# Performance work log

Hardware: AMD Instinct MI355X
Metric: run time of the kernel (lower is better)

The kernel has to match this reference:

```python
import math
import jax, jax.numpy as jnp
import numpy as np

BATCH, SEQ, D_MODEL, NUM_HEADS = 4, 2048, 1024, 16
D_K = D_MODEL // NUM_HEADS


def setup_inputs() -> dict:
    key = jax.random.key(0)
    ks = jax.random.split(key, 11)
    s = 0.02
    inp = {
        'encodings_q': jax.random.normal(ks[0], (BATCH, SEQ, D_MODEL), jnp.float32),
        'encodings_k': jax.random.normal(ks[1], (BATCH, SEQ, D_MODEL), jnp.float32),
        'encodings_v': jax.random.normal(ks[2], (BATCH, SEQ, D_MODEL), jnp.float32),
        # causal mask: True = masked out (matches masked_fill semantics)
        'mask': jnp.broadcast_to(jnp.triu(jnp.ones((SEQ, SEQ), bool), k=1),
                                 (BATCH, SEQ, SEQ)),
        'Wq': jax.random.normal(ks[3], (D_MODEL, D_MODEL), jnp.float32) * s,
        'bq': jnp.zeros((D_MODEL,), jnp.float32),
        'Wk': jax.random.normal(ks[4], (D_MODEL, D_MODEL), jnp.float32) * s,
        'bk': jnp.zeros((D_MODEL,), jnp.float32),
        'Wv': jax.random.normal(ks[5], (D_MODEL, D_MODEL), jnp.float32) * s,
        'bv': jnp.zeros((D_MODEL,), jnp.float32),
        'Wo': jax.random.normal(ks[6], (D_MODEL, D_MODEL), jnp.float32) * s,
        'bo': jnp.zeros((D_MODEL,), jnp.float32),
    }
    return inp


def reference(encodings_q, encodings_k, encodings_v, mask,
              Wq, bq, Wk, bk, Wv, bv, Wo, bo):
    B, S, D = encodings_q.shape
    H, Dk = NUM_HEADS, D_K
    # projections (nn.Linear: x @ W.T + b), split heads -> (B, H, S, Dk)
    q = (encodings_q @ Wq.T + bq).reshape(B, S, H, Dk).transpose(0, 2, 1, 3)
    k = (encodings_k @ Wk.T + bk).reshape(B, S, H, Dk).transpose(0, 2, 1, 3)
    v = (encodings_v @ Wv.T + bv).reshape(B, S, H, Dk).transpose(0, 2, 1, 3)
    scores = jnp.einsum('bhqd,bhkd->bhqk', q, k) / math.sqrt(Dk)
    # mask dim == 3 -> unsqueeze head dim; masked_fill(mask, -1e9)
    scores = jnp.where(mask[:, None, :, :], jnp.float32(-1e9), scores)
    weights = jax.nn.softmax(scores, axis=-1)
    attn = jnp.einsum('bhqk,bhkd->bhqd', weights, v)
    attn = attn.transpose(0, 2, 1, 3).reshape(B, S, D)
    return attn @ Wo.T + bo
```

## Files before the change

kernel.cpp:

```cpp
#include <hip/hip_runtime.h>
#include <hip/hip_bf16.h>
#include <cstdint>

typedef __bf16 bf16;
typedef bf16  bf16x4 __attribute__((ext_vector_type(4)));
typedef bf16  bf16x8 __attribute__((ext_vector_type(8)));
typedef float f32x4  __attribute__((ext_vector_type(4)));

#define MFMA16(a, b, c) __builtin_amdgcn_mfma_f32_16x16x32_bf16((a), (b), (c), 0, 0, 0)

constexpr int BATCH = 4;
constexpr int SEQ   = 2048;
constexpr int DM    = 1024;
constexpr int NH    = 16;
constexpr int DK    = 64;

constexpr float QSCALE = 0.125f * 1.44269504088896340736f;

__device__ __forceinline__ void gld_lds16(const void* g, void* l) {
    __builtin_amdgcn_global_load_lds(
        (const __attribute__((address_space(1))) unsigned int*)(uintptr_t)g,
        (__attribute__((address_space(3))) unsigned int*)(uintptr_t)l,
        16, 0, 0);
}

__device__ __forceinline__ bf16x8 cvt8(const float* __restrict__ p) {
    f32x4 a = *(const f32x4*)p;
    f32x4 b = *(const f32x4*)(p + 4);
    bf16x8 r;
    r[0] = (bf16)a[0]; r[1] = (bf16)a[1]; r[2] = (bf16)a[2]; r[3] = (bf16)a[3];
    r[4] = (bf16)b[0]; r[5] = (bf16)b[1]; r[6] = (bf16)b[2]; r[7] = (bf16)b[3];
    return r;
}

__global__ __launch_bounds__(256)
void cvt_all(const float* __restrict__ xq, const float* __restrict__ xk,
             const float* __restrict__ xv,
             const float* __restrict__ wq, const float* __restrict__ wk,
             const float* __restrict__ wv, const float* __restrict__ wo,
             bf16* __restrict__ X3, bf16* __restrict__ WB)
{
    const int bid = blockIdx.x;
    const float* s;
    bf16* d;
    int local;
    if (bid < 12288) {
        const int which = bid >> 12;
        local = bid & 4095;
        s = (which == 0) ? xq : (which == 1) ? xk : xv;
        d = X3 + (size_t)which * ((size_t)BATCH * SEQ * DM);
    } else {
        const int b2 = bid - 12288;
        const int which = b2 >> 9;
        local = b2 & 511;
        s = (which == 0) ? wq : (which == 1) ? wk : (which == 2) ? wv : wo;
        d = WB + (size_t)which * (size_t)(DM * DM);
    }
    const size_t i = ((size_t)local * 256 + threadIdx.x) * 8;
    *(bf16x8*)(d + i) = cvt8(s + i);
}

__global__ __launch_bounds__(256)
void cvt_x(const float* __restrict__ src, bf16* __restrict__ dst) {
    const size_t i = ((size_t)blockIdx.x * 256 + threadIdx.x) * 8;
    *(bf16x8*)(dst + i) = cvt8(src + i);
}

__global__ __launch_bounds__(256)
void cvt_w4(const float* __restrict__ s0, const float* __restrict__ s1,
            const float* __restrict__ s2, const float* __restrict__ s3,
            bf16* __restrict__ dst) {
    const float* s = (blockIdx.y == 0) ? s0 : (blockIdx.y == 1) ? s1
                   : (blockIdx.y == 2) ? s2 : s3;
    const size_t i = ((size_t)blockIdx.x * 256 + threadIdx.x) * 8;
    *(bf16x8*)(dst + (size_t)blockIdx.y * (1024 * 1024) + i) = cvt8(s + i);
}

template <int MODE>
__device__ __forceinline__
void gemm_core(const bf16* __restrict__ A, const bf16* __restrict__ W,
               const float* __restrict__ bias, void* __restrict__ outp,
               int m0, int n0, bf16* As, bf16* Bs, float oscale)
{
    const int tid  = threadIdx.x;
    const int lane = tid & 63;
    const int wave = tid >> 6;
    const int wm   = (wave >> 1) * 64;
    const int wn   = (wave & 1) * 64;
    const int q4   = lane >> 4;
    const int r    = lane & 15;
    const int srow = lane >> 2;
    const int scol = (lane & 3) * 8;

    f32x4 acc[4][4];
#pragma unroll
    for (int i = 0; i < 4; i++)
#pragma unroll
        for (int j = 0; j < 4; j++) acc[i][j] = (f32x4){0.f, 0.f, 0.f, 0.f};

    const bf16* Ag = A + (size_t)(m0 + wave * 32 + srow) * 1024 + scol;
    const bf16* Wg = W + (size_t)(n0 + wave * 32 + srow) * 1024 + scol;
    const int woff = (wave * 32) * 32;
    constexpr int BUF = 128 * 32;

    gld_lds16(Ag,             As + woff);
    gld_lds16(Ag + 16 * 1024, As + woff + 16 * 32);
    gld_lds16(Wg,             Bs + woff);
    gld_lds16(Wg + 16 * 1024, Bs + woff + 16 * 32);

    int cur = 0;
    for (int k0 = 0; k0 < 1024; k0 += 32) {
        __syncthreads();

        if (k0 < 1024 - 32) {
            const int nb = (cur ^ 1) * BUF + woff;
            gld_lds16(Ag + k0 + 32,             As + nb);
            gld_lds16(Ag + k0 + 32 + 16 * 1024, As + nb + 16 * 32);
            gld_lds16(Wg + k0 + 32,             Bs + nb);
            gld_lds16(Wg + k0 + 32 + 16 * 1024, Bs + nb + 16 * 32);
        }

        const bf16* Ar = As + cur * BUF;
        const bf16* Br = Bs + cur * BUF;

        bf16x8 af[4], bfr[4];
#pragma unroll
        for (int i = 0; i < 4; i++)
            af[i] = *(const bf16x8*)&Ar[(wm + i * 16 + r) * 32 + q4 * 8];
#pragma unroll
        for (int j = 0; j < 4; j++)
            bfr[j] = *(const bf16x8*)&Br[(wn + j * 16 + r) * 32 + q4 * 8];
#pragma unroll
        for (int i = 0; i < 4; i++)
#pragma unroll
            for (int j = 0; j < 4; j++) {
                if (MODE == 2)
                    acc[i][j] = MFMA16(af[i], bfr[j], acc[i][j]);
                else
                    acc[i][j] = MFMA16(bfr[j], af[i], acc[i][j]);
            }
        cur ^= 1;
    }

    if (MODE == 2) {
#pragma unroll
        for (int j = 0; j < 4; j++) {
            const int col = n0 + wn + j * 16 + r;
            const float bv = bias[col];
            const int hh = col >> 6, d = col & 63;
#pragma unroll
            for (int i = 0; i < 4; i++) {
                const int s0 = m0 + wm + i * 16 + q4 * 4;
                const int b = s0 >> 11, s = s0 & 2047;
                bf16x4 ov;
#pragma unroll
                for (int rr = 0; rr < 4; rr++) ov[rr] = (bf16)((acc[i][j][rr] + bv) * oscale);
                *(bf16x4*)&((bf16*)outp)[(((size_t)(b * NH + hh)) * DK + d) * SEQ + s] = ov;
            }
        }
    } else {
#pragma unroll
        for (int j = 0; j < 4; j++) {
            const int col0 = n0 + wn + j * 16 + q4 * 4;
            const f32x4 bv4 = *(const f32x4*)&bias[col0];
#pragma unroll
            for (int i = 0; i < 4; i++) {
                const int row = m0 + wm + i * 16 + r;
                if (MODE == 1) {
                    f32x4 ov = (acc[i][j] + bv4) * oscale;
                    *(f32x4*)&((float*)outp)[(size_t)row * 1024 + col0] = ov;
                } else {
                    const int b = row >> 11, s = row & 2047;
                    const int hh = col0 >> 6, d0 = col0 & 63;
                    bf16x4 ov;
#pragma unroll
                    for (int rr = 0; rr < 4; rr++) ov[rr] = (bf16)((acc[i][j][rr] + bv4[rr]) * oscale);
                    *(bf16x4*)&((bf16*)outp)[(((size_t)(b * NH + hh)) * SEQ + s) * DK + d0] = ov;
                }
            }
        }
    }
}

template <int MODE>
__global__ __launch_bounds__(256)
void gemm_fast(const bf16* __restrict__ A, const bf16* __restrict__ W,
               const float* __restrict__ bias, void* __restrict__ outp, float oscale)
{
    __shared__ __align__(16) bf16 As[2][128 * 32];
    __shared__ __align__(16) bf16 Bs[2][128 * 32];
    gemm_core<MODE>(A, W, bias, outp, blockIdx.x * 128, blockIdx.y * 128,
                    &As[0][0], &Bs[0][0], oscale);
}

__global__ __launch_bounds__(256)
void gemm_qkv(const bf16* __restrict__ X3, const bf16* __restrict__ WB,
              const float* __restrict__ bq, const float* __restrict__ bk,
              const float* __restrict__ bv,
              bf16* __restrict__ Qt, bf16* __restrict__ Kt, bf16* __restrict__ Vt)
{
    __shared__ __align__(16) bf16 As[2][128 * 32];
    __shared__ __align__(16) bf16 Bs[2][128 * 32];
    const int z = blockIdx.z;
    const size_t E = (size_t)BATCH * SEQ * DM, WE = (size_t)DM * DM;
    const bf16* A = X3 + (size_t)z * E;
    const bf16* W = WB + (size_t)z * WE;
    const int m0 = blockIdx.x * 128, n0 = blockIdx.y * 128;
    if (z == 2)
        gemm_core<2>(A, W, bv, Vt, m0, n0, &As[0][0], &Bs[0][0], 1.0f);
    else if (z == 1)
        gemm_core<0>(A, W, bk, Kt, m0, n0, &As[0][0], &Bs[0][0], 1.0f);
    else
        gemm_core<0>(A, W, bq, Qt, m0, n0, &As[0][0], &Bs[0][0], QSCALE);
}

template <int MODE>
__global__ __launch_bounds__(256)
void gemm_slow(const void* __restrict__ Ap, const float* __restrict__ W,
               const float* __restrict__ bias, void* __restrict__ outp, float oscale)
{
    __shared__ __align__(16) bf16 As[128 * 32];
    __shared__ __align__(16) bf16 Bs[128 * 32];

    const int tid  = threadIdx.x;
    const int lane = tid & 63;
    const int wave = tid >> 6;
    const int wm   = (wave >> 1) * 64;
    const int wn   = (wave & 1) * 64;
    const int m0   = blockIdx.y * 128;
    const int n0   = blockIdx.x * 128;
    const int q    = lane >> 4;
    const int r    = lane & 15;
    const int lrow  = tid >> 2;
    const int lcol8 = (tid & 3) * 8;

    f32x4 acc[4][4];
#pragma unroll
    for (int i = 0; i < 4; i++)
#pragma unroll
        for (int j = 0; j < 4; j++) acc[i][j] = (f32x4){0.f, 0.f, 0.f, 0.f};

    for (int k0 = 0; k0 < 1024; k0 += 32) {
        __syncthreads();
        if (MODE != 1) {
            const float* Af = (const float*)Ap;
            *(bf16x8*)&As[lrow * 32 + lcol8] =
                cvt8(&Af[(size_t)(m0 + lrow) * 1024 + k0 + lcol8]);
            *(bf16x8*)&As[(64 + lrow) * 32 + lcol8] =
                cvt8(&Af[(size_t)(m0 + 64 + lrow) * 1024 + k0 + lcol8]);
        } else {
            const bf16* Ab = (const bf16*)Ap;
            *(bf16x8*)&As[lrow * 32 + lcol8] =
                *(const bf16x8*)&Ab[(size_t)(m0 + lrow) * 1024 + k0 + lcol8];
            *(bf16x8*)&As[(64 + lrow) * 32 + lcol8] =
                *(const bf16x8*)&Ab[(size_t)(m0 + 64 + lrow) * 1024 + k0 + lcol8];
        }
        *(bf16x8*)&Bs[lrow * 32 + lcol8] =
            cvt8(&W[(size_t)(n0 + lrow) * 1024 + k0 + lcol8]);
        *(bf16x8*)&Bs[(64 + lrow) * 32 + lcol8] =
            cvt8(&W[(size_t)(n0 + 64 + lrow) * 1024 + k0 + lcol8]);
        __syncthreads();

        bf16x8 af[4], bfr[4];
#pragma unroll
        for (int i = 0; i < 4; i++)
            af[i] = *(const bf16x8*)&As[(wm + i * 16 + r) * 32 + q * 8];
#pragma unroll
        for (int j = 0; j < 4; j++)
            bfr[j] = *(const bf16x8*)&Bs[(wn + j * 16 + r) * 32 + q * 8];
#pragma unroll
        for (int i = 0; i < 4; i++)
#pragma unroll
            for (int j = 0; j < 4; j++)
                acc[i][j] = MFMA16(af[i], bfr[j], acc[i][j]);
    }

#pragma unroll
    for (int j = 0; j < 4; j++) {
        const int col = n0 + wn + j * 16 + r;
        const float bv = bias[col];
#pragma unroll
        for (int i = 0; i < 4; i++) {
#pragma unroll
            for (int rr = 0; rr < 4; rr++) {
                const int row = m0 + wm + i * 16 + q * 4 + rr;
                const float v = (acc[i][j][rr] + bv) * oscale;
                if (MODE == 1) {
                    ((float*)outp)[(size_t)row * 1024 + col] = v;
                } else {
                    const int b = row >> 11, s = row & 2047;
                    const int hh = col >> 6, d = col & 63;
                    if (MODE == 0)
                        ((bf16*)outp)[(((size_t)(b * NH + hh)) * SEQ + s) * DK + d] = (bf16)v;
                    else
                        ((bf16*)outp)[(((size_t)(b * NH + hh)) * DK + d) * SEQ + s] = (bf16)v;
                }
            }
        }
    }
}

__global__ __launch_bounds__(256)
void attn_causal(const bf16* __restrict__ Qt, const bf16* __restrict__ Kt,
                 const bf16* __restrict__ Vtt, bf16* __restrict__ Ob)
{
    __shared__ __align__(16) bf16 Ks[2][64 * 64];
    __shared__ __align__(16) bf16 Vs[2][64 * 64];
    __shared__ __align__(16) bf16 Ps[4][16 * 64];

    const int tid  = threadIdx.x;
    const int lane = tid & 63;
    const int wave = tid >> 6;
    const int q4   = lane >> 4;
    const int r    = lane & 15;

    const int bh = blockIdx.x;
    const int yy = (SEQ / 64 - 1) - blockIdx.y;
    const int qb = yy * 64;
    const int b  = bh >> 4;
    const int h  = bh & 15;

    const bf16* Qp = Qt  + ((size_t)bh * SEQ + qb + wave * 16) * DK;
    const bf16* Kp = Kt  + (size_t)bh * SEQ * DK;
    const bf16* Vp = Vtt + (size_t)bh * DK * SEQ;

    const bf16x8 qf0 = *(const bf16x8*)&Qp[r * DK + q4 * 8];
    const bf16x8 qf1 = *(const bf16x8*)&Qp[r * DK + 32 + q4 * 8];

    bf16x8 ones;
#pragma unroll
    for (int j = 0; j < 8; j++) ones[j] = (bf16)1.0f;

    f32x4 o[4], o5;
#pragma unroll
    for (int i = 0; i < 4; i++) o[i] = (f32x4){0.f, 0.f, 0.f, 0.f};
    o5 = (f32x4){0.f, 0.f, 0.f, 0.f};
    float m_i = -1e30f;

    const int nT   = yy + 1;
    const int qrow = qb + wave * 16 + r;

    const int srow = wave * 16 + (lane >> 3);
    const int scol = ((lane & 7) ^ (srow & 7)) * 8;
    const bf16* KgA = Kp + (size_t)srow * DK + scol;
    const bf16* VgA = Vp + (size_t)srow * SEQ + scol;

    const int sw    = r & 7;
    const int koffA = r * 64 + ((q4)     ^ sw) * 8;
    const int koffB = r * 64 + ((q4 + 4) ^ sw) * 8;

    const int pwr = r * 64;

    {
        bf16* kd = &Ks[0][wave * 1024];
        bf16* vd = &Vs[0][wave * 1024];
        gld_lds16(KgA,           kd);
        gld_lds16(KgA + 8 * DK,  kd + 512);
        gld_lds16(VgA,           vd);
        gld_lds16(VgA + 8 * SEQ, vd + 512);
        KgA += 64 * DK;
        VgA += 64;
    }

    int nbuf = 0;
    for (int t = 0; t < nT; ++t) {
        __syncthreads();

        const bf16* Kb = Ks[nbuf];
        const bf16* Vb = Vs[nbuf];

        if (t + 1 < nT) {
            bf16* kd = &Ks[nbuf ^ 1][wave * 1024];
            bf16* vd = &Vs[nbuf ^ 1][wave * 1024];
            gld_lds16(KgA,           kd);
            gld_lds16(KgA + 8 * DK,  kd + 512);
            gld_lds16(VgA,           vd);
            gld_lds16(VgA + 8 * SEQ, vd + 512);
            KgA += 64 * DK;
            VgA += 64;
        }

        f32x4 s[4];
        __builtin_amdgcn_s_setprio(1);
#pragma unroll
        for (int n = 0; n < 4; n++) {
            bf16x8 k0 = *(const bf16x8*)&Kb[koffA + n * 1024];
            bf16x8 k1 = *(const bf16x8*)&Kb[koffB + n * 1024];
            f32x4 a = (f32x4){0.f, 0.f, 0.f, 0.f};
            a = MFMA16(k0, qf0, a);
            a = MFMA16(k1, qf1, a);
            s[n] = a;
        }
        __builtin_amdgcn_s_setprio(0);

        const int kb = t * 64;
        float mx = -1e30f;
        if (t == nT - 1) {
#pragma unroll
            for (int n = 0; n < 4; n++) {
                const int c0 = kb + n * 16 + q4 * 4;
#pragma unroll
                for (int rr = 0; rr < 4; rr++) {
                    if (c0 + rr > qrow) s[n][rr] = -1e30f;
                    mx = fmaxf(mx, s[n][rr]);
                }
            }
        } else {
#pragma unroll
            for (int n = 0; n < 4; n++)
#pragma unroll
                for (int rr = 0; rr < 4; rr++)
                    mx = fmaxf(mx, s[n][rr]);
        }
        mx = fmaxf(mx, __shfl_xor(mx, 16, 64));
        mx = fmaxf(mx, __shfl_xor(mx, 32, 64));

        if (__any(mx > m_i + 8.0f)) {
            const float mn    = fmaxf(m_i, mx);
            const float alpha = __builtin_amdgcn_exp2f(m_i - mn);
            m_i = mn;
#pragma unroll
            for (int n = 0; n < 4; n++)
#pragma unroll
                for (int rr = 0; rr < 4; rr++)
                    o[n][rr] *= alpha;
#pragma unroll
            for (int rr = 0; rr < 4; rr++) o5[rr] *= alpha;
        }

        bf16* Pw = &Ps[wave][0];
#pragma unroll
        for (int n = 0; n < 4; n++) {
            bf16x4 pv;
#pragma unroll
            for (int rr = 0; rr < 4; rr++)
                pv[rr] = (bf16)__builtin_amdgcn_exp2f(s[n][rr] - m_i);
            *(bf16x4*)&Pw[pwr + (((n * 4 + q4) ^ ((r & 7) << 1)) << 2)] = pv;
        }
        asm volatile("s_waitcnt lgkmcnt(0)" ::: "memory");

        __builtin_amdgcn_s_setprio(1);
#pragma unroll
        for (int kk = 0; kk < 2; kk++) {
            bf16x8 pf = *(const bf16x8*)&Pw[pwr + (((kk * 4 + q4) ^ (r & 7)) << 3)];
            const int vo = (kk == 0) ? koffA : koffB;
#pragma unroll
            for (int n = 0; n < 4; n++) {
                bf16x8 vf = *(const bf16x8*)&Vb[vo + n * 1024];
                o[n] = MFMA16(vf, pf, o[n]);
            }
            o5 = MFMA16(ones, pf, o5);
        }
        __builtin_amdgcn_s_setprio(0);

        nbuf ^= 1;
    }

    const float inv = 1.0f / o5[0];
#pragma unroll
    for (int n = 0; n < 4; n++) {
        bf16x4 ov;
#pragma unroll
        for (int rr = 0; rr < 4; rr++) ov[rr] = (bf16)(o[n][rr] * inv);
        *(bf16x4*)&Ob[((size_t)b * SEQ + qrow) * DM + h * DK + n * 16 + q4 * 4] = ov;
    }
}

extern "C" void kernel_launch(void* const* d_in, const int* in_sizes, int n_in,
                              void* d_out, int out_size, void* d_ws, size_t ws_size,
                              hipStream_t stream)
{
    const float* xq = (const float*)d_in[0];
    const float* xk = (const float*)d_in[1];
    const float* xv = (const float*)d_in[2];
    const float* Wq = (const float*)d_in[4];
    const float* bq = (const float*)d_in[5];
    const float* Wk = (const float*)d_in[6];
    const float* bk = (const float*)d_in[7];
    const float* Wv = (const float*)d_in[8];
    const float* bv = (const float*)d_in[9];
    const float* Wo = (const float*)d_in[10];
    const float* bo = (const float*)d_in[11];

    const size_t E  = (size_t)BATCH * SEQ * DM;
    const size_t WE = (size_t)DM * DM;
    bf16* Qt = (bf16*)d_ws;
    bf16* Kt = Qt + E;
    bf16* Vt = Kt + E;
    bf16* Ab = Vt + E;

    dim3 gblk(256);
    dim3 agrid(BATCH * NH, SEQ / 64);

    const size_t need_fused = (7 * E + 4 * WE) * sizeof(bf16);
    const size_t need_fast  = (5 * E + 4 * WE) * sizeof(bf16);

    if (ws_size >= need_fused) {
        bf16* X3 = Ab + E;
        bf16* WB = X3 + 3 * E;

        cvt_all<<<dim3(14336), gblk, 0, stream>>>(xq, xk, xv, Wq, Wk, Wv, Wo, X3, WB);

        gemm_qkv<<<dim3(64, 8, 3), gblk, 0, stream>>>(X3, WB, bq, bk, bv, Qt, Kt, Vt);

        attn_causal<<<agrid, gblk, 0, stream>>>(Qt, Kt, Vt, Ab);

        gemm_fast<1><<<dim3(64, 8), gblk, 0, stream>>>(Ab, WB + 3 * WE, bo, d_out, 1.0f);
    } else if (ws_size >= need_fast) {
        bf16* X  = Ab + E;
        bf16* WB = X + E;

        cvt_w4<<<dim3(512, 4), gblk, 0, stream>>>(Wq, Wk, Wv, Wo, WB);

        cvt_x<<<dim3(4096), gblk, 0, stream>>>(xq, X);
        gemm_fast<0><<<dim3(64, 8), gblk, 0, stream>>>(X, WB + 0 * WE, bq, Qt, QSCALE);
        cvt_x<<<dim3(4096), gblk, 0, stream>>>(xk, X);
        gemm_fast<0><<<dim3(64, 8), gblk, 0, stream>>>(X, WB + 1 * WE, bk, Kt, 1.0f);
        cvt_x<<<dim3(4096), gblk, 0, stream>>>(xv, X);
        gemm_fast<2><<<dim3(64, 8), gblk, 0, stream>>>(X, WB + 2 * WE, bv, Vt, 1.0f);

        attn_causal<<<agrid, gblk, 0, stream>>>(Qt, Kt, Vt, Ab);

        gemm_fast<1><<<dim3(64, 8), gblk, 0, stream>>>(Ab, WB + 3 * WE, bo, d_out, 1.0f);
    } else {
        dim3 ggrid_s(DM / 128, (BATCH * SEQ) / 128);
        gemm_slow<0><<<ggrid_s, gblk, 0, stream>>>(xq, Wq, bq, Qt, QSCALE);
        gemm_slow<0><<<ggrid_s, gblk, 0, stream>>>(xk, Wk, bk, Kt, 1.0f);
        gemm_slow<2><<<ggrid_s, gblk, 0, stream>>>(xv, Wv, bv, Vt, 1.0f);
        attn_causal<<<agrid, gblk, 0, stream>>>(Qt, Kt, Vt, Ab);
        gemm_slow<1><<<ggrid_s, gblk, 0, stream>>>(Ab, Wo, bo, d_out, 1.0f);
    }
}
```

Baseline: 349.5 us.

## Triple-buffer GEMM LDS staging with explicit vmcnt waits

```diff
diff --git a/kernel.cpp b/kernel.cpp
--- a/kernel.cpp
+++ b/kernel.cpp
@@ -103,22 +103,27 @@
     const int woff = (wave * 32) * 32;
     constexpr int BUF = 128 * 32;
 
-    gld_lds16(Ag,             As + woff);
-    gld_lds16(Ag + 16 * 1024, As + woff + 16 * 32);
-    gld_lds16(Wg,             Bs + woff);
-    gld_lds16(Wg + 16 * 1024, Bs + woff + 16 * 32);
-
-    int cur = 0;
-    for (int k0 = 0; k0 < 1024; k0 += 32) {
-        __syncthreads();
-
-        if (k0 < 1024 - 32) {
-            const int nb = (cur ^ 1) * BUF + woff;
-            gld_lds16(Ag + k0 + 32,             As + nb);
-            gld_lds16(Ag + k0 + 32 + 16 * 1024, As + nb + 16 * 32);
-            gld_lds16(Wg + k0 + 32,             Bs + nb);
-            gld_lds16(Wg + k0 + 32 + 16 * 1024, Bs + nb + 16 * 32);
-        }
+#define GSTAGE(ks, bsel) do {                                        \
+        const int _b = (bsel) * BUF + woff;                          \
+        gld_lds16(Ag + (ks) * 32,             As + _b);              \
+        gld_lds16(Ag + (ks) * 32 + 16 * 1024, As + _b + 16 * 32);   \
+        gld_lds16(Wg + (ks) * 32,             Bs + _b);              \
+        gld_lds16(Wg + (ks) * 32 + 16 * 1024, Bs + _b + 16 * 32);   \
+    } while (0)
+
+    GSTAGE(0, 0);
+    GSTAGE(1, 1);
+
+    int cur = 0, pre = 2;
+    for (int t = 0; t < 32; ++t) {
+        if (t < 30) {
+            asm volatile("s_waitcnt vmcnt(4) lgkmcnt(0)" ::: "memory");
+        } else {
+            asm volatile("s_waitcnt vmcnt(0) lgkmcnt(0)" ::: "memory");
+        }
+        __builtin_amdgcn_s_barrier();
+
+        if (t < 30) GSTAGE(t + 2, pre);
 
         const bf16* Ar = As + cur * BUF;
         const bf16* Br = Bs + cur * BUF;
@@ -139,8 +144,11 @@
                 else
                     acc[i][j] = MFMA16(bfr[j], af[i], acc[i][j]);
             }
-        cur ^= 1;
-    }
+
+        cur = (cur == 2) ? 0 : cur + 1;
+        pre = (pre == 2) ? 0 : pre + 1;
+    }
+#undef GSTAGE
 
     if (MODE == 2) {
 #pragma unroll
@@ -187,8 +195,8 @@
 void gemm_fast(const bf16* __restrict__ A, const bf16* __restrict__ W,
                const float* __restrict__ bias, void* __restrict__ outp, float oscale)
 {
-    __shared__ __align__(16) bf16 As[2][128 * 32];
-    __shared__ __align__(16) bf16 Bs[2][128 * 32];
+    __shared__ __align__(16) bf16 As[3][128 * 32];
+    __shared__ __align__(16) bf16 Bs[3][128 * 32];
     gemm_core<MODE>(A, W, bias, outp, blockIdx.x * 128, blockIdx.y * 128,
                     &As[0][0], &Bs[0][0], oscale);
 }
@@ -199,8 +207,8 @@
               const float* __restrict__ bv,
               bf16* __restrict__ Qt, bf16* __restrict__ Kt, bf16* __restrict__ Vt)
 {
-    __shared__ __align__(16) bf16 As[2][128 * 32];
-    __shared__ __align__(16) bf16 Bs[2][128 * 32];
+    __shared__ __align__(16) bf16 As[3][128 * 32];
+    __shared__ __align__(16) bf16 Bs[3][128 * 32];
     const int z = blockIdx.z;
     const size_t E = (size_t)BATCH * SEQ * DM, WE = (size_t)DM * DM;
     const bf16* A = X3 + (size_t)z * E;
```

Result: no change. 344.8 us (-1.3%).
